# Kernel tuning notes

Hardware: AMD Instinct MI355X
Metric: run time of the kernel (lower is better)

Reference implementation:

```python
import jax, jax.numpy as jnp
import numpy as np

B, S, D, H = 2, 2048, 512, 8


def setup_inputs() -> dict:
    key = jax.random.key(0)
    ks = jax.random.split(key, 9)
    scale = 1.0 / np.sqrt(D)
    x = jax.random.normal(ks[0], (B, S, D), dtype=jnp.float32)
    # Per-head full-width projections, stacked over heads: [H, D, D]
    Wq = jax.random.normal(ks[1], (H, D, D), dtype=jnp.float32) * scale
    Wk = jax.random.normal(ks[2], (H, D, D), dtype=jnp.float32) * scale
    Wv = jax.random.normal(ks[3], (H, D, D), dtype=jnp.float32) * scale
    bq = jax.random.normal(ks[4], (H, D), dtype=jnp.float32) * 0.01
    bk = jax.random.normal(ks[5], (H, D), dtype=jnp.float32) * 0.01
    bv = jax.random.normal(ks[6], (H, D), dtype=jnp.float32) * 0.01
    Wo = jax.random.normal(ks[7], (H * D, D), dtype=jnp.float32) * (1.0 / np.sqrt(H * D))
    bo = jax.random.normal(ks[8], (D,), dtype=jnp.float32) * 0.01
    return {"x": x, "Wq": Wq, "bq": bq, "Wk": Wk, "bk": bk, "Wv": Wv, "bv": bv, "Wo": Wo, "bo": bo}


def reference(x, Wq, bq, Wk, bk, Wv, bv, Wo, bo):
    # Batched per-head projections: [B,S,D] x [H,D,E] -> [B,H,S,E]
    q = jnp.einsum('bsd,hde->bhse', x, Wq) + bq[None, :, None, :]
    k = jnp.einsum('bsd,hde->bhse', x, Wk) + bk[None, :, None, :]
    v = jnp.einsum('bsd,hde->bhse', x, Wv) + bv[None, :, None, :]
    # NOTE: original module has NO 1/sqrt(d) scaling
    scores = jnp.einsum('bhse,bhte->bhst', q, k)  # [B,H,S,S]
    attn = jax.nn.softmax(scores, axis=-1)
    out = jnp.einsum('bhst,bhte->bhse', attn, v)  # [B,H,S,D]
    # Concat heads along feature dim: [B,S,H*D]
    cat = out.transpose(0, 2, 1, 3).reshape(B, S, H * D)
    return cat @ Wo + bo
```

## Files before the change

### kernel.cpp

```cpp
#include <hip/hip_runtime.h>

typedef _Float16 f16;
typedef _Float16 f16x8 __attribute__((ext_vector_type(8)));
typedef float f32x4 __attribute__((ext_vector_type(4)));

#define B_ 2
#define S_ 2048
#define D_ 512
#define H_ 8

__device__ inline void async_ld16(const void* g, void* l) {
  __builtin_amdgcn_global_load_lds((__attribute__((address_space(1))) void*)(g),
                                   (__attribute__((address_space(3))) void*)(l),
                                   16, 0, 0);
}

__device__ inline unsigned fmap(float f) {
  unsigned u = __float_as_uint(f);
  return (u & 0x80000000u) ? ~u : (u | 0x80000000u);
}
__device__ inline float funmap(unsigned k) {
  return (k & 0x80000000u) ? __uint_as_float(k ^ 0x80000000u) : __uint_as_float(~k);
}

__global__ __launch_bounds__(256) void cvt_f16(const float* __restrict__ src,
                                               f16* __restrict__ dst, long n) {
  long i = (long)blockIdx.x * 256 + threadIdx.x;
  if (i >= n) return;
  dst[i] = (f16)src[i];
}

__global__ __launch_bounds__(256) void transpose_f32(const float* __restrict__ src,
                                                     f16* __restrict__ dst, int R, int C) {
  __shared__ float t[32][33];
  size_t zoff = (size_t)blockIdx.z * R * C;
  const float* s = src + zoff;
  int tx = threadIdx.x;
  int ty = threadIdx.y;
  int c0 = blockIdx.x * 32, r0 = blockIdx.y * 32;
#pragma unroll
  for (int i = 0; i < 4; ++i)
    t[ty + i * 8][tx] = s[(size_t)(r0 + ty + i * 8) * C + c0 + tx];
  __syncthreads();
#pragma unroll
  for (int i = 0; i < 4; ++i)
    dst[zoff + (size_t)(c0 + ty + i * 8) * R + r0 + tx] = (f16)t[tx][ty + i * 8];
}

__global__ __launch_bounds__(256) void reduce_out(const float* __restrict__ part,
                                                  const float* __restrict__ bo,
                                                  float* __restrict__ out, long n, int nslab) {
  long i = (long)blockIdx.x * 256 + threadIdx.x;
  if (i >= n) return;
  float v = bo[i & (D_ - 1)];
  for (int s = 0; s < nslab; ++s) v += part[(long)s * n + i];
  out[i] = v;
}

struct GemmArgs {
  const f16 *A, *Bm;
  void* C;
  const float* bias;
  unsigned* Mout;
  float* Mloc;
  int K, lda, ldb, ldc;
  int zbase, NG, PBG;
  long sAp, sAb, sAg, sAz;
  long sBp, sBb, sBg, sBz;
  long sCp, sCb, sCg, sCz;
  long sbp, sbb, sbg, sbz;
  long sMz, sMlz;
};

template <typename OutT, int BIAS, bool PEXP>
__global__ __launch_bounds__(256) void gemm_nt(GemmArgs p) {
  int zloc = blockIdx.z;
  int zi = p.zbase + zloc;
  int pp = zi / p.PBG; int rz = zi - pp * p.PBG;
  int bb = rz / p.NG;  int g = rz - bb * p.NG;
  const f16* A  = p.A + (pp * p.sAp + bb * p.sAb + g * p.sAg + (long)zloc * p.sAz);
  const f16* Bm = p.Bm + (pp * p.sBp + bb * p.sBb + g * p.sBg + (long)zloc * p.sBz);
  OutT* C = (OutT*)p.C + (pp * p.sCp + bb * p.sCb + g * p.sCg + (long)zloc * p.sCz);
  const float* bias = nullptr;
  if (BIAS) bias = p.bias + (pp * p.sbp + bb * p.sbb + g * p.sbg + (long)zloc * p.sbz);
  unsigned* Mz = PEXP ? (p.Mout + (long)zloc * p.sMz) : nullptr;

  __shared__ f16 lA[4096];
  __shared__ f16 lB[4096];
  __shared__ float lMx[PEXP ? 256 : 1];
  __shared__ f16 lR[PEXP ? 32 * 136 : 1];

  int tid = threadIdx.x;
  int lane = tid & 63;
  int w = tid >> 6;
  int wm = (w >> 1) << 6;
  int wn = (w & 1) << 6;
  long bm = (long)blockIdx.y * 128;
  long bn = (long)blockIdx.x * 128;

  f32x4 acc[4][4] = {};
  int qd = lane >> 4;
  int fr = lane & 15;

  int q0 = tid, q1 = tid + 256;
  int r0s = q0 >> 2, c0s = (q0 & 3) ^ ((r0s >> 1) & 3);
  int r1s = q1 >> 2, c1s = (q1 & 3) ^ ((r1s >> 1) & 3);

  for (int k0 = 0; k0 < p.K; k0 += 32) {
    long oa0 = (bm + r0s) * (long)p.lda + (k0 + c0s * 8);
    long oa1 = (bm + r1s) * (long)p.lda + (k0 + c1s * 8);
    long ob0 = (bn + r0s) * (long)p.ldb + (k0 + c0s * 8);
    long ob1 = (bn + r1s) * (long)p.ldb + (k0 + c1s * 8);
    __syncthreads();
    async_ld16(A + oa0,  lA + (size_t)q0 * 8);
    async_ld16(A + oa1,  lA + (size_t)q1 * 8);
    async_ld16(Bm + ob0, lB + (size_t)q0 * 8);
    async_ld16(Bm + ob1, lB + (size_t)q1 * 8);
    __syncthreads();

    f16x8 ah[4], bh[4];
#pragma unroll
    for (int i = 0; i < 4; ++i) {
      int m = wm + i * 16 + fr;
      ah[i] = *(const f16x8*)(lA + ((size_t)m * 4 + (qd ^ ((m >> 1) & 3))) * 8);
      int n = wn + i * 16 + fr;
      bh[i] = *(const f16x8*)(lB + ((size_t)n * 4 + (qd ^ ((n >> 1) & 3))) * 8);
    }
#pragma unroll
    for (int i = 0; i < 4; ++i)
#pragma unroll
      for (int j = 0; j < 4; ++j)
        acc[i][j] = __builtin_amdgcn_mfma_f32_16x16x32_f16(ah[i], bh[j], acc[i][j], 0, 0, 0);
  }

  int rr0 = qd * 4;
  if (PEXP) {
#pragma unroll
    for (int i = 0; i < 4; ++i) {
#pragma unroll
      for (int r = 0; r < 4; ++r) {
        float v = fmaxf(fmaxf(acc[i][0][r], acc[i][1][r]),
                        fmaxf(acc[i][2][r], acc[i][3][r]));
        v = fmaxf(v, __shfl_xor(v, 1, 64));
        v = fmaxf(v, __shfl_xor(v, 2, 64));
        v = fmaxf(v, __shfl_xor(v, 4, 64));
        v = fmaxf(v, __shfl_xor(v, 8, 64));
        if (fr == 0) lMx[(w & 1) * 128 + wm + i * 16 + rr0 + r] = v;
      }
    }
    __syncthreads();
    if (tid < 128) {
      float ml = fmaxf(lMx[tid], lMx[128 + tid]);
      long row = bm + tid;
      p.Mloc[(long)zloc * p.sMlz + (long)blockIdx.x * S_ + row] = ml;
      atomicMax(Mz + row, fmap(ml));
    }
    int rowBase = (w >> 1) << 4;
#pragma unroll
    for (int i = 0; i < 4; ++i) {
      __syncthreads();
#pragma unroll
      for (int r = 0; r < 4; ++r) {
        int rl = wm + i * 16 + rr0 + r;
        float ml = fmaxf(lMx[rl], lMx[128 + rl]);
        int rowLoc = rowBase + rr0 + r;
#pragma unroll
        for (int j = 0; j < 4; ++j) {
          int col = wn + j * 16 + fr;
          lR[rowLoc * 136 + col] = (f16)__expf(acc[i][j][r] - ml);
        }
      }
      __syncthreads();
      int rowLoc = tid >> 3;
      int colLoc = (tid & 7) * 16;
      long grow = bm + ((rowLoc & 15) + i * 16) + ((long)(rowLoc >> 4) << 6);
      f16x8 v0 = *(const f16x8*)(lR + rowLoc * 136 + colLoc);
      f16x8 v1 = *(const f16x8*)(lR + rowLoc * 136 + colLoc + 8);
      f16* dst = (f16*)C + grow * (long)p.ldc + bn + colLoc;
      *(f16x8*)(dst) = v0;
      *(f16x8*)(dst + 8) = v1;
    }
  } else {
#pragma unroll
    for (int i = 0; i < 4; ++i) {
#pragma unroll
      for (int j = 0; j < 4; ++j) {
#pragma unroll
        for (int r = 0; r < 4; ++r) {
          long row = bm + wm + i * 16 + rr0 + r;
          long col = bn + wn + j * 16 + fr;
          float v = acc[i][j][r];
          if (BIAS == 1) v += bias[col];
          if (BIAS == 2) v += bias[row];
          C[row * (long)p.ldc + col] = (OutT)v;
        }
      }
    }
  }
}

struct PvArgs {
  const f16* S; const unsigned* M; const float* Ml; const f16* V; f16* C;
  int ldc, zbase, NG;
  long sVz, sCb, sCg;
};
__global__ __launch_bounds__(256) void pv_flash(PvArgs p) {
  int zloc = blockIdx.z;
  int zi = p.zbase + zloc;
  int bb = zi / p.NG; int g = zi - bb * p.NG;
  const f16* Sm = p.S + (long)zloc * S_ * S_;
  const unsigned* Mz = p.M + (long)zloc * S_;
  const float* Ml = p.Ml + (long)zloc * 16 * S_;
  const f16* V = p.V + (long)zloc * p.sVz;
  f16* C = p.C + bb * p.sCb + g * p.sCg;

  __shared__ f16 lP[64 * 32];
  __shared__ f16 lV[256 * 32];

  int tid = threadIdx.x;
  int lane = tid & 63;
  int w = tid >> 6;
  long bm = (long)blockIdx.y * 64;
  long bn = (long)blockIdx.x * 256;
  int e0 = w << 6;

  int qd = lane >> 4;
  int fr = lane & 15;

  f32x4 acc[4][4] = {};
  f32x4 lacc[4] = {};
  f16x8 ones;
#pragma unroll
  for (int j = 0; j < 8; ++j) ones[j] = (f16)1.0f;

  float mg[4];
#pragma unroll
  for (int i = 0; i < 4; ++i) mg[i] = funmap(Mz[bm + i * 16 + fr]);
  f16 al16[4];

  int rs = tid >> 2, cs = (tid & 3) ^ ((rs >> 1) & 3);

  for (int k0 = 0; k0 < S_; k0 += 32) {
    if ((k0 & 127) == 0) {
      int cb = k0 >> 7;
#pragma unroll
      for (int i = 0; i < 4; ++i)
        al16[i] = (f16)__expf(Ml[cb * S_ + bm + i * 16 + fr] - mg[i]);
    }
    __syncthreads();
    async_ld16(Sm + (bm + rs) * (long)S_ + (k0 + cs * 8), lP + (size_t)tid * 8);
#pragma unroll
    for (int j = 0; j < 4; ++j) {
      int q = j * 256 + tid;
      int rv = q >> 2, cv = (q & 3) ^ ((rv >> 1) & 3);
      async_ld16(V + (bn + rv) * (long)S_ + (k0 + cv * 8), lV + (size_t)q * 8);
    }
    __syncthreads();

    f16x8 ah[4], bh[4];
#pragma unroll
    for (int i = 0; i < 4; ++i) {
      int m = i * 16 + fr;
      ah[i] = *(const f16x8*)(lP + ((size_t)m * 4 + (qd ^ ((m >> 1) & 3))) * 8);
#pragma unroll
      for (int j = 0; j < 8; ++j) ah[i][j] *= al16[i];
    }
#pragma unroll
    for (int j = 0; j < 4; ++j) {
      int n = e0 + j * 16 + fr;
      bh[j] = *(const f16x8*)(lV + ((size_t)n * 4 + (qd ^ ((n >> 1) & 3))) * 8);
    }
#pragma unroll
    for (int i = 0; i < 4; ++i) {
      lacc[i] = __builtin_amdgcn_mfma_f32_16x16x32_f16(ah[i], ones, lacc[i], 0, 0, 0);
#pragma unroll
      for (int j = 0; j < 4; ++j)
        acc[i][j] = __builtin_amdgcn_mfma_f32_16x16x32_f16(ah[i], bh[j], acc[i][j], 0, 0, 0);
    }
  }

  int rr0 = (lane >> 4) * 4;
#pragma unroll
  for (int i = 0; i < 4; ++i) {
    float inv[4];
#pragma unroll
    for (int r = 0; r < 4; ++r) inv[r] = 1.0f / lacc[i][r];
#pragma unroll
    for (int j = 0; j < 4; ++j) {
#pragma unroll
      for (int r = 0; r < 4; ++r) {
        long row = bm + i * 16 + rr0 + r;
        long col = bn + e0 + j * 16 + fr;
        C[row * (long)p.ldc + col] = (f16)(acc[i][j][r] * inv[r]);
      }
    }
  }
}

extern "C" void kernel_launch(void* const* d_in, const int* in_sizes, int n_in,
                              void* d_out, int out_size, void* d_ws, size_t ws_size,
                              hipStream_t stream) {
  const float* x  = (const float*)d_in[0];
  const float* Wq = (const float*)d_in[1];
  const float* bq = (const float*)d_in[2];
  const float* Wk = (const float*)d_in[3];
  const float* bk = (const float*)d_in[4];
  const float* Wv = (const float*)d_in[5];
  const float* bv = (const float*)d_in[6];
  const float* Wo = (const float*)d_in[7];
  const float* bo = (const float*)d_in[8];
  float* out = (float*)d_out;

  auto al = [](size_t v) { return (v + 255) & ~(size_t)255; };
  const size_t eX = (size_t)B_ * S_ * D_;
  const size_t eW = (size_t)H_ * D_ * D_;
  const size_t eSS = (size_t)S_ * S_;
  const long SD = (long)S_ * D_;
  const long DD = (long)D_ * D_;
  const long DS = (long)D_ * S_;

  size_t fixed = al(eX * 2) + al(2 * eW * 2) + al(eW * 2) + al(eW * 2)
               + al(2ULL * H_ * D_ * 4);
  int NB = 1, GH = 1, GS = 1; bool found = false;
  for (int nb = 2; nb >= 1 && !found; --nb)
    for (int gh = 8; gh >= 1 && !found; gh >>= 1)
      for (int gs = nb * gh; gs >= 1 && !found; gs >>= 1) {
        size_t need = fixed + al((size_t)nb * S_ * H_ * D_ * 2)
                    + al(2ULL * nb * gh * S_ * D_ * 2)
                    + al((size_t)nb * gh * D_ * S_ * 2)
                    + al(4ULL * nb * SD * 4)
                    + al((size_t)gs * eSS * 2) + al((size_t)gs * S_ * 4)
                    + al((size_t)gs * 16 * S_ * 4);
        if (need <= ws_size) { NB = nb; GH = gh; GS = gs; found = true; }
      }

  char* p0 = (char*)d_ws;
  size_t off = 0;
  f16* xh    = (f16*)(p0 + off); off += al(eX * 2);
  f16* wqk   = (f16*)(p0 + off); off += al(2 * eW * 2);
  f16* wv    = (f16*)(p0 + off); off += al(eW * 2);
  f16* wo    = (f16*)(p0 + off); off += al(eW * 2);
  float* bqk = (float*)(p0 + off); off += al(2ULL * H_ * D_ * 4);
  f16* catb  = (f16*)(p0 + off); off += al((size_t)NB * S_ * H_ * D_ * 2);
  f16* qk    = (f16*)(p0 + off); off += al(2ULL * NB * GH * S_ * D_ * 2);
  f16* vT    = (f16*)(p0 + off); off += al((size_t)NB * GH * D_ * S_ * 2);
  float* opart = (float*)(p0 + off); off += al(4ULL * NB * SD * 4);
  f16* scores = (f16*)(p0 + off); off += al((size_t)GS * eSS * 2);
  unsigned* rowmax = (unsigned*)(p0 + off); off += al((size_t)GS * S_ * 4);
  float* mloc = (float*)(p0 + off);

  cvt_f16<<<dim3((unsigned)((eX + 255) / 256)), 256, 0, stream>>>(x, xh, (long)eX);
  dim3 tb(32, 8, 1);
  transpose_f32<<<dim3(16, 16, H_), tb, 0, stream>>>(Wq, wqk, D_, D_);
  transpose_f32<<<dim3(16, 16, H_), tb, 0, stream>>>(Wk, wqk + eW, D_, D_);
  transpose_f32<<<dim3(16, 16, H_), tb, 0, stream>>>(Wv, wv, D_, D_);
  transpose_f32<<<dim3(16, 128, 1), tb, 0, stream>>>(Wo, wo, H_ * D_, D_);
  hipMemcpyAsync(bqk, bq, (size_t)H_ * D_ * 4, hipMemcpyDeviceToDevice, stream);
  hipMemcpyAsync(bqk + H_ * D_, bk, (size_t)H_ * D_ * 4, hipMemcpyDeviceToDevice, stream);

  for (int b0 = 0; b0 < B_; b0 += NB) {
    for (int h0 = 0; h0 < H_; h0 += GH) {
      {
        GemmArgs a{};
        a.A = xh + (long)b0 * SD;
        a.Bm = wqk + (long)h0 * DD;
        a.C = qk; a.bias = bqk + (long)h0 * D_;
        a.K = D_; a.lda = D_; a.ldb = D_; a.ldc = D_;
        a.zbase = 0; a.NG = GH; a.PBG = NB * GH;
        a.sAb = SD;
        a.sBp = (long)H_ * DD; a.sBg = DD;
        a.sCz = SD;
        a.sbp = (long)H_ * D_; a.sbg = D_;
        gemm_nt<f16, 1, false><<<dim3(4, 16, 2 * NB * GH), 256, 0, stream>>>(a);
      }
      {
        GemmArgs a{};
        a.A = wv + (long)h0 * DD; a.Bm = xh + (long)b0 * SD;
        a.C = vT; a.bias = bv + (long)h0 * D_;
        a.K = D_; a.lda = D_; a.ldb = D_; a.ldc = S_;
        a.zbase = 0; a.NG = GH; a.PBG = NB * GH;
        a.sAg = DD;
        a.sBb = SD;
        a.sCz = DS;
        a.sbg = D_;
        gemm_nt<f16, 2, false><<<dim3(16, 4, NB * GH), 256, 0, stream>>>(a);
      }
      for (int g0 = 0; g0 < NB * GH; g0 += GS) {
        hipMemsetAsync(rowmax, 0, (size_t)GS * S_ * 4, stream);
        {
          GemmArgs a{};
          a.A = qk + (long)g0 * SD;
          a.Bm = qk + ((long)NB * GH + g0) * SD;
          a.C = scores; a.Mout = rowmax; a.Mloc = mloc;
          a.K = D_; a.lda = D_; a.ldb = D_; a.ldc = S_;
          a.zbase = g0; a.NG = GH; a.PBG = NB * GH;
          a.sAz = SD; a.sBz = SD; a.sCz = (long)eSS; a.sMz = S_;
          a.sMlz = 16L * S_;
          gemm_nt<f16, 0, true><<<dim3(16, 16, GS), 256, 0, stream>>>(a);
        }
        {
          PvArgs a{};
          a.S = scores; a.M = rowmax; a.Ml = mloc; a.V = vT + (long)g0 * DS;
          a.C = catb + (long)h0 * D_;
          a.ldc = H_ * D_; a.zbase = g0; a.NG = GH;
          a.sVz = DS; a.sCb = (long)S_ * H_ * D_; a.sCg = D_;
          pv_flash<<<dim3(2, S_ / 64, GS), 256, 0, stream>>>(a);
        }
      }
    }
    {
      GemmArgs a{};
      a.A = catb; a.Bm = wo;
      a.C = opart;
      a.K = 1024; a.lda = H_ * D_; a.ldb = H_ * D_; a.ldc = D_;
      a.zbase = 0; a.NG = 4; a.PBG = NB * 4;
      a.sAb = (long)S_ * H_ * D_; a.sAg = 1024;
      a.sBg = 1024;
      a.sCb = SD; a.sCg = (long)NB * SD;
      gemm_nt<float, 0, false><<<dim3(4, 16, NB * 4), 256, 0, stream>>>(a);
    }
    reduce_out<<<dim3((unsigned)(((long)NB * SD + 255) / 256)), 256, 0, stream>>>(
        opart, bo, out + (long)b0 * SD, (long)NB * SD, 4);
  }
}
```

Before: 520.8 us.

## Fuse Q/K/V projection GEMMs into one launch and shrink PV tile width

Adds a qkv_proj kernel that computes the Q, K and V^T projections for all batches and heads in a single launch, replacing the two separate gemm_nt launches when NB==2 and GH==8. The PV flash kernel's N tile is halved from 256 to 128 columns, with the grid doubled to match. This gives more blocks, less LDS and fewer accumulators per thread, at the cost of reading the P tile and recomputing the row sums twice as often. Whether the fused path runs depends on NB and GH values that are not shown.

New measurement: 527.3 us. About the same (+1.3%).

```diff
diff --git a/kernel.cpp b/kernel.cpp
--- a/kernel.cpp
+++ b/kernel.cpp
@@ -199,6 +199,100 @@
   }
 }
 
+struct QkvArgs {
+  const f16 *xh, *wqk, *wv;
+  f16 *qk, *vT;
+  const float *bqk, *bv;
+};
+__global__ __launch_bounds__(256) void qkv_proj(QkvArgs p) {
+  const long SD = (long)S_ * D_, DD = (long)D_ * D_, DS = (long)D_ * S_;
+  int zi = blockIdx.z;
+  int pp = zi >> 4;
+  int r = zi & 15;
+  int b = r >> 3, h = r & 7;
+  int bid = blockIdx.x;
+  const f16 *A, *Bm;
+  f16* C;
+  const float* bias;
+  long bm, bn;
+  int ldc;
+  bool biasRow;
+  if (pp < 2) {
+    A = p.xh + (long)b * SD;
+    Bm = p.wqk + ((long)pp * 8 + h) * DD;
+    C = p.qk + (long)zi * SD;
+    bias = p.bqk + ((long)pp * 8 + h) * D_;
+    bm = (long)(bid >> 2) * 128; bn = (long)(bid & 3) * 128;
+    ldc = D_; biasRow = false;
+  } else {
+    A = p.wv + (long)h * DD;
+    Bm = p.xh + (long)b * SD;
+    C = p.vT + (long)(b * 8 + h) * DS;
+    bias = p.bv + (long)h * D_;
+    bm = (long)(bid >> 4) * 128; bn = (long)(bid & 15) * 128;
+    ldc = S_; biasRow = true;
+  }
+
+  __shared__ f16 lA[4096];
+  __shared__ f16 lB[4096];
+
+  int tid = threadIdx.x;
+  int lane = tid & 63;
+  int w = tid >> 6;
+  int wm = (w >> 1) << 6;
+  int wn = (w & 1) << 6;
+
+  f32x4 acc[4][4] = {};
+  int qd = lane >> 4;
+  int fr = lane & 15;
+
+  int q0 = tid, q1 = tid + 256;
+  int r0s = q0 >> 2, c0s = (q0 & 3) ^ ((r0s >> 1) & 3);
+  int r1s = q1 >> 2, c1s = (q1 & 3) ^ ((r1s >> 1) & 3);
+
+  for (int k0 = 0; k0 < D_; k0 += 32) {
+    long oa0 = (bm + r0s) * (long)D_ + (k0 + c0s * 8);
+    long oa1 = (bm + r1s) * (long)D_ + (k0 + c1s * 8);
+    long ob0 = (bn + r0s) * (long)D_ + (k0 + c0s * 8);
+    long ob1 = (bn + r1s) * (long)D_ + (k0 + c1s * 8);
+    __syncthreads();
+    async_ld16(A + oa0,  lA + (size_t)q0 * 8);
+    async_ld16(A + oa1,  lA + (size_t)q1 * 8);
+    async_ld16(Bm + ob0, lB + (size_t)q0 * 8);
+    async_ld16(Bm + ob1, lB + (size_t)q1 * 8);
+    __syncthreads();
+
+    f16x8 ah[4], bh[4];
+#pragma unroll
+    for (int i = 0; i < 4; ++i) {
+      int m = wm + i * 16 + fr;
+      ah[i] = *(const f16x8*)(lA + ((size_t)m * 4 + (qd ^ ((m >> 1) & 3))) * 8);
+      int n = wn + i * 16 + fr;
+      bh[i] = *(const f16x8*)(lB + ((size_t)n * 4 + (qd ^ ((n >> 1) & 3))) * 8);
+    }
+#pragma unroll
+    for (int i = 0; i < 4; ++i)
+#pragma unroll
+      for (int j = 0; j < 4; ++j)
+        acc[i][j] = __builtin_amdgcn_mfma_f32_16x16x32_f16(ah[i], bh[j], acc[i][j], 0, 0, 0);
+  }
+
+  int rr0 = qd * 4;
+#pragma unroll
+  for (int i = 0; i < 4; ++i) {
+#pragma unroll
+    for (int j = 0; j < 4; ++j) {
+#pragma unroll
+      for (int r = 0; r < 4; ++r) {
+        long row = bm + wm + i * 16 + rr0 + r;
+        long col = bn + wn + j * 16 + fr;
+        float v = acc[i][j][r] + (biasRow ? bias[row] : bias[col]);
+        C[row * (long)ldc + col] = (f16)v;
+      }
+    }
+  }
+}
+
 struct PvArgs {
   const f16* S; const unsigned* M; const float* Ml; const f16* V; f16* C;
   int ldc, zbase, NG;
@@ -215,19 +309,19 @@
   f16* C = p.C + bb * p.sCb + g * p.sCg;
 
   __shared__ f16 lP[64 * 32];
-  __shared__ f16 lV[256 * 32];
+  __shared__ f16 lV[128 * 32];
 
   int tid = threadIdx.x;
   int lane = tid & 63;
   int w = tid >> 6;
   long bm = (long)blockIdx.y * 64;
-  long bn = (long)blockIdx.x * 256;
-  int e0 = w << 6;
+  long bn = (long)blockIdx.x * 128;
+  int e0 = w << 5;
 
   int qd = lane >> 4;
   int fr = lane & 15;
 
-  f32x4 acc[4][4] = {};
+  f32x4 acc[4][2] = {};
   f32x4 lacc[4] = {};
   f16x8 ones;
 #pragma unroll
@@ -239,6 +333,7 @@
   f16 al16[4];
 
   int rs = tid >> 2, cs = (tid & 3) ^ ((rs >> 1) & 3);
+  int rv1 = (tid + 256) >> 2, cv1 = ((tid + 256) & 3) ^ ((rv1 >> 1) & 3);
 
   for (int k0 = 0; k0 < S_; k0 += 32) {
     if ((k0 & 127) == 0) {
@@ -249,15 +344,11 @@
     }
     __syncthreads();
     async_ld16(Sm + (bm + rs) * (long)S_ + (k0 + cs * 8), lP + (size_t)tid * 8);
-#pragma unroll
-    for (int j = 0; j < 4; ++j) {
-      int q = j * 256 + tid;
-      int rv = q >> 2, cv = (q & 3) ^ ((rv >> 1) & 3);
-      async_ld16(V + (bn + rv) * (long)S_ + (k0 + cv * 8), lV + (size_t)q * 8);
-    }
-    __syncthreads();
-
-    f16x8 ah[4], bh[4];
+    async_ld16(V + (bn + rs) * (long)S_ + (k0 + cs * 8), lV + (size_t)tid * 8);
+    async_ld16(V + (bn + rv1) * (long)S_ + (k0 + cv1 * 8), lV + (size_t)(tid + 256) * 8);
+    __syncthreads();
+
+    f16x8 ah[4], bh[2];
 #pragma unroll
     for (int i = 0; i < 4; ++i) {
       int m = i * 16 + fr;
@@ -266,7 +357,7 @@
       for (int j = 0; j < 8; ++j) ah[i][j] *= al16[i];
     }
 #pragma unroll
-    for (int j = 0; j < 4; ++j) {
+    for (int j = 0; j < 2; ++j) {
       int n = e0 + j * 16 + fr;
       bh[j] = *(const f16x8*)(lV + ((size_t)n * 4 + (qd ^ ((n >> 1) & 3))) * 8);
     }
@@ -274,7 +365,7 @@
     for (int i = 0; i < 4; ++i) {
       lacc[i] = __builtin_amdgcn_mfma_f32_16x16x32_f16(ah[i], ones, lacc[i], 0, 0, 0);
 #pragma unroll
-      for (int j = 0; j < 4; ++j)
+      for (int j = 0; j < 2; ++j)
         acc[i][j] = __builtin_amdgcn_mfma_f32_16x16x32_f16(ah[i], bh[j], acc[i][j], 0, 0, 0);
     }
   }
@@ -286,7 +377,7 @@
 #pragma unroll
     for (int r = 0; r < 4; ++r) inv[r] = 1.0f / lacc[i][r];
 #pragma unroll
-    for (int j = 0; j < 4; ++j) {
+    for (int j = 0; j < 2; ++j) {
 #pragma unroll
       for (int r = 0; r < 4; ++r) {
         long row = bm + i * 16 + rr0 + r;
@@ -360,30 +451,35 @@
 
   for (int b0 = 0; b0 < B_; b0 += NB) {
     for (int h0 = 0; h0 < H_; h0 += GH) {
-      {
-        GemmArgs a{};
-        a.A = xh + (long)b0 * SD;
-        a.Bm = wqk + (long)h0 * DD;
-        a.C = qk; a.bias = bqk + (long)h0 * D_;
-        a.K = D_; a.lda = D_; a.ldb = D_; a.ldc = D_;
-        a.zbase = 0; a.NG = GH; a.PBG = NB * GH;
-        a.sAb = SD;
-        a.sBp = (long)H_ * DD; a.sBg = DD;
-        a.sCz = SD;
-        a.sbp = (long)H_ * D_; a.sbg = D_;
-        gemm_nt<f16, 1, false><<<dim3(4, 16, 2 * NB * GH), 256, 0, stream>>>(a);
-      }
-      {
-        GemmArgs a{};
-        a.A = wv + (long)h0 * DD; a.Bm = xh + (long)b0 * SD;
-        a.C = vT; a.bias = bv + (long)h0 * D_;
-        a.K = D_; a.lda = D_; a.ldb = D_; a.ldc = S_;
-        a.zbase = 0; a.NG = GH; a.PBG = NB * GH;
-        a.sAg = DD;
-        a.sBb = SD;
-        a.sCz = DS;
-        a.sbg = D_;
-        gemm_nt<f16, 2, false><<<dim3(16, 4, NB * GH), 256, 0, stream>>>(a);
+      if (NB == 2 && GH == 8) {
+        QkvArgs a{xh, wqk, wv, qk, vT, bqk, bv};
+        qkv_proj<<<dim3(64, 1, 48), 256, 0, stream>>>(a);
+      } else {
+        {
+          GemmArgs a{};
+          a.A = xh + (long)b0 * SD;
+          a.Bm = wqk + (long)h0 * DD;
+          a.C = qk; a.bias = bqk + (long)h0 * D_;
+          a.K = D_; a.lda = D_; a.ldb = D_; a.ldc = D_;
+          a.zbase = 0; a.NG = GH; a.PBG = NB * GH;
+          a.sAb = SD;
+          a.sBp = (long)H_ * DD; a.sBg = DD;
+          a.sCz = SD;
+          a.sbp = (long)H_ * D_; a.sbg = D_;
+          gemm_nt<f16, 1, false><<<dim3(4, 16, 2 * NB * GH), 256, 0, stream>>>(a);
+        }
+        {
+          GemmArgs a{};
+          a.A = wv + (long)h0 * DD; a.Bm = xh + (long)b0 * SD;
+          a.C = vT; a.bias = bv + (long)h0 * D_;
+          a.K = D_; a.lda = D_; a.ldb = D_; a.ldc = S_;
+          a.zbase = 0; a.NG = GH; a.PBG = NB * GH;
+          a.sAg = DD;
+          a.sBb = SD;
+          a.sCz = DS;
+          a.sbg = D_;
+          gemm_nt<f16, 2, false><<<dim3(16, 4, NB * GH), 256, 0, stream>>>(a);
+        }
       }
       for (int g0 = 0; g0 < NB * GH; g0 += GS) {
         hipMemsetAsync(rowmax, 0, (size_t)GS * S_ * 4, stream);
@@ -404,7 +500,7 @@
           a.C = catb + (long)h0 * D_;
           a.ldc = H_ * D_; a.zbase = g0; a.NG = GH;
           a.sVz = DS; a.sCb = (long)S_ * H_ * D_; a.sCg = D_;
-          pv_flash<<<dim3(2, S_ / 64, GS), 256, 0, stream>>>(a);
+          pv_flash<<<dim3(4, S_ / 64, GS), 256, 0, stream>>>(a);
         }
       }
     }
```
